# Optimization experiments

Measured on AMD Instinct MI355X. Metric: run time of the kernel, lower is better.

## Reference

```python
import jax, jax.numpy as jnp
import numpy as np

B, N, D, E, K = 4, 4096, 2048, 128, 8


def setup_inputs() -> dict:
    key = jax.random.key(0)
    kx, kw, kb = jax.random.split(key, 3)
    x = jax.random.normal(kx, (B, N, D), dtype=jnp.float32)
    # nn.Linear(input_dim, num_experts): weight [E, D], bias [E]
    bound = 1.0 / np.sqrt(D)
    W = jax.random.uniform(kw, (E, D), dtype=jnp.float32, minval=-bound, maxval=bound)
    b = jax.random.uniform(kb, (E,), dtype=jnp.float32, minval=-bound, maxval=bound)
    return {"x": x, "W": W, "b": b}


def reference(x, W, b):
    # gate logits: [B, N, E]
    gate_logits = jnp.einsum("bnd,ed->bne", x, W) + b
    # top-k over experts
    topk_values, topk_indices = jax.lax.top_k(gate_logits, K)  # [B,N,K]
    topk_gates = jax.nn.softmax(topk_values, axis=-1)          # [B,N,K]
    # scatter normalized gates back into dense [B,N,E]
    onehot = jax.nn.one_hot(topk_indices, E, dtype=topk_gates.dtype)  # [B,N,K,E]
    full_gates = jnp.einsum("bnke,bnk->bne", onehot, topk_gates)
    return full_gates, topk_indices
```

## Files before the change

kernel.cpp:

```cpp
#include <hip/hip_runtime.h>
#include <cfloat>

#define TOKENS 16384
#define DDIM   2048
#define NEXP   128
#define KTOP   8
#define MB     64
#define CH     64
#define NCH    (DDIM / CH)
#define NTHR   512

typedef float    f32x4 __attribute__((ext_vector_type(4)));
typedef _Float16 f16x8 __attribute__((ext_vector_type(8)));

#define WFRAG_N (8 * NCH * 2 * 64)

__device__ __forceinline__ unsigned short f16bits(float f) {
    _Float16 h = (_Float16)f;
    return __builtin_bit_cast(unsigned short, h);
}
__device__ __forceinline__ float f16tof(unsigned short u) {
    return (float)__builtin_bit_cast(_Float16, u);
}

__global__ __launch_bounds__(256, 1) void wfrag_kernel(
    const float* __restrict__ W, uint4* __restrict__ wf)
{
    int id   = blockIdx.x * 256 + threadIdx.x;
    int lane = id & 63;
    int ks   = (id >> 6) & 1;
    int c    = (id >> 7) & (NCH - 1);
    int eb   = id >> 12;
    int e    = eb * 16 + (lane & 15);
    int k0   = c * CH + ks * 32 + (lane >> 4) * 8;
    const float4* src = (const float4*)(W + (size_t)e * DDIM + k0);
    float4 a = src[0], bq = src[1];
    float v[8] = {a.x, a.y, a.z, a.w, bq.x, bq.y, bq.z, bq.w};
    unsigned hw[4], mw[4];
#pragma unroll
    for (int p = 0; p < 4; ++p) {
        unsigned short h0 = f16bits(v[2 * p]), h1 = f16bits(v[2 * p + 1]);
        unsigned short m0 = f16bits((v[2 * p]     - f16tof(h0)) * 4096.0f);
        unsigned short m1 = f16bits((v[2 * p + 1] - f16tof(h1)) * 4096.0f);
        hw[p] = (unsigned)h0 | ((unsigned)h1 << 16);
        mw[p] = (unsigned)m0 | ((unsigned)m1 << 16);
    }
    wf[id]           = make_uint4(hw[0], hw[1], hw[2], hw[3]);
    wf[WFRAG_N + id] = make_uint4(mw[0], mw[1], mw[2], mw[3]);
}

__device__ __forceinline__ void insert8(float (&vals)[8], int (&idxs)[8], float v, int e) {
    bool c[8];
#pragma unroll
    for (int p = 0; p < 8; ++p) c[p] = v > vals[p];
#pragma unroll
    for (int p = 7; p >= 1; --p) {
        vals[p] = c[p] ? (c[p - 1] ? vals[p - 1] : v) : vals[p];
        idxs[p] = c[p] ? (c[p - 1] ? idxs[p - 1] : e) : idxs[p];
    }
    vals[0] = c[0] ? v : vals[0];
    idxs[0] = c[0] ? e : idxs[0];
}

__device__ __forceinline__ void chunk_barrier() {
    asm volatile("s_waitcnt lgkmcnt(0)" ::: "memory");
    __builtin_amdgcn_sched_barrier(0);
    __builtin_amdgcn_s_barrier();
    __builtin_amdgcn_sched_barrier(0);
}

__global__ __launch_bounds__(NTHR, 1) void router_kernel(
    const float* __restrict__ x, const uint4* __restrict__ wf,
    const float* __restrict__ b, float* __restrict__ out_gates,
    float* __restrict__ out_idx)
{
    __shared__ __align__(16) char smem[52224];
    float* lg  = (float*)smem;
    float* plv = (float*)(smem + 33792);
    int*   pli = (int*)(smem + 43008);

    const int tid  = threadIdx.x;
    const int lane = tid & 63;
    const int wid  = tid >> 6;
    const int tok0 = blockIdx.x * MB;

    const uint4* WFH = wf;
    const uint4* WFM = wf + WFRAG_N;

    f32x4 acc1[4], acc2[4];
#pragma unroll
    for (int mf = 0; mf < 4; ++mf) {
        acc1[mf] = (f32x4){0.f, 0.f, 0.f, 0.f};
        acc2[mf] = (f32x4){0.f, 0.f, 0.f, 0.f};
    }

    const float4* x4 = (const float4*)x;
    const int xr0 = tid >> 4, xr1 = 32 + (tid >> 4), xq = tid & 15;
    const size_t xoff0 = (size_t)(tok0 + xr0) * (DDIM / 4) + xq;
    const size_t xoff1 = (size_t)(tok0 + xr1) * (DDIM / 4) + xq;
    const int xb0 = xr0 * 128 + (((xq >> 1) ^ (xr0 & 7)) << 4) + (xq & 1) * 8;
    const int xb1 = xr1 * 128 + (((xq >> 1) ^ (xr1 & 7)) << 4) + (xq & 1) * 8;

    float4 S0[2], S1[2], S2[2], S3[2], S4[2], S5[2], S6[2], S7[2];
    uint4  wA[4], wB[4];

    auto loadX = [&](int c, float4 (&S)[2]) {
        S[0] = x4[xoff0 + (size_t)c * 16];
        S[1] = x4[xoff1 + (size_t)c * 16];
    };
    auto loadW = [&](int c, uint4 (&wreg)[4]) {
#pragma unroll
        for (int ks = 0; ks < 2; ++ks) {
            int idx = ((wid * NCH + c) * 2 + ks) * 64 + lane;
            wreg[ks]     = WFH[idx];
            wreg[2 + ks] = WFM[idx];
        }
    };
    auto convertX = [&](const float4 (&sx)[2], char* ldsDst) {
#pragma unroll
        for (int r = 0; r < 2; ++r) {
            const float4 v = sx[r];
            unsigned short h0 = f16bits(v.x), h1 = f16bits(v.y);
            unsigned short h2 = f16bits(v.z), h3 = f16bits(v.w);
            unsigned short m0 = f16bits((v.x - f16tof(h0)) * 4096.0f);
            unsigned short m1 = f16bits((v.y - f16tof(h1)) * 4096.0f);
            unsigned short m2 = f16bits((v.z - f16tof(h2)) * 4096.0f);
            unsigned short m3 = f16bits((v.w - f16tof(h3)) * 4096.0f);
            uint2 hv = make_uint2((unsigned)h0 | ((unsigned)h1 << 16),
                                  (unsigned)h2 | ((unsigned)h3 << 16));
            uint2 mv = make_uint2((unsigned)m0 | ((unsigned)m1 << 16),
                                  (unsigned)m2 | ((unsigned)m3 << 16));
            const int byteoff = r ? xb1 : xb0;
            *(uint2*)(ldsDst + byteoff)         = hv;
            *(uint2*)(ldsDst + 16384 + byteoff) = mv;
        }
    };

    auto step = [&](int c, float4 (&Sload)[2], float4 (&Scvt)[2],
                    uint4 (&wCur)[4], uint4 (&wNext)[4],
                    char* bufCur, char* bufNext) {
        if (c + 8 < NCH) loadX(c + 8, Sload);
        if (c + 1 < NCH) loadW(c + 1, wNext);

#pragma unroll
        for (int ks = 0; ks < 2; ++ks) {
            f16x8 ah[4], am[4];
#pragma unroll
            for (int mf = 0; mf < 4; ++mf) {
                int row = 16 * mf + (lane & 15);
                int byteoff = row * 128 +
                    ((((ks << 2) | (lane >> 4)) ^ (row & 7)) << 4);
                ah[mf] = *(const f16x8*)(bufCur + byteoff);
                am[mf] = *(const f16x8*)(bufCur + 16384 + byteoff);
            }
            f16x8 wh = __builtin_bit_cast(f16x8, wCur[ks]);
            f16x8 wm = __builtin_bit_cast(f16x8, wCur[2 + ks]);
#pragma unroll
            for (int mf = 0; mf < 4; ++mf) {
                acc1[mf] = __builtin_amdgcn_mfma_f32_16x16x32_f16(
                    ah[mf], wh, acc1[mf], 0, 0, 0);
                acc2[mf] = __builtin_amdgcn_mfma_f32_16x16x32_f16(
                    ah[mf], wm, acc2[mf], 0, 0, 0);
                acc2[mf] = __builtin_amdgcn_mfma_f32_16x16x32_f16(
                    am[mf], wh, acc2[mf], 0, 0, 0);
            }
        }

        if (c + 1 < NCH) convertX(Scvt, bufNext);
        chunk_barrier();
    };

    loadX(0, S0);
    loadX(1, S1);
    loadW(0, wA);
    loadX(2, S2);
    loadX(3, S3);
    loadX(4, S4);
    loadX(5, S5);
    loadX(6, S6);
    loadX(7, S7);
    convertX(S0, smem);
    chunk_barrier();

    char* buf0 = smem;
    char* buf1 = smem + 8192;
    for (int cc = 0; cc < NCH; cc += 8) {
        step(cc,     S0, S1, wA, wB, buf0, buf1);
        step(cc + 1, S1, S2, wB, wA, buf1, buf0);
        step(cc + 2, S2, S3, wA, wB, buf0, buf1);
        step(cc + 3, S3, S4, wB, wA, buf1, buf0);
        step(cc + 4, S4, S5, wA, wB, buf0, buf1);
        step(cc + 5, S5, S6, wB, wA, buf1, buf0);
        step(cc + 6, S6, S7, wA, wB, buf0, buf1);
        step(cc + 7, S7, S0, wB, wA, buf1, buf0);
    }

    const float bb = b[wid * 16 + (lane & 15)];
#pragma unroll
    for (int mf = 0; mf < 4; ++mf)
#pragma unroll
        for (int r = 0; r < 4; ++r) {
            int t = 16 * mf + (lane >> 4) * 4 + r;
            int e = wid * 16 + (lane & 15);
            lg[t * 132 + e] =
                fmaf(acc2[mf][r], 0.000244140625f, acc1[mf][r]) + bb;
        }
    __syncthreads();

    if (tid < 256) {
        int tt = tid >> 2, p = tid & 3;
        float vals[8]; int idxs[8];
#pragma unroll
        for (int k = 0; k < 8; ++k) { vals[k] = -FLT_MAX; idxs[k] = 0; }
        const float* row = &lg[tt * 132 + p * 32];
        for (int q = 0; q < 32; ++q)
            insert8(vals, idxs, row[q], p * 32 + q);
#pragma unroll
        for (int k = 0; k < 8; ++k) {
            plv[tid * 9 + k] = vals[k];
            pli[tid * 9 + k] = idxs[k];
        }
    }
    __syncthreads();

    float g[8]; int fidx[8];
    const bool active = (tid < MB);
    if (active) {
        float vals[8]; int idxs[8];
#pragma unroll
        for (int k = 0; k < 8; ++k) { vals[k] = -FLT_MAX; idxs[k] = 0; }
        for (int p = 0; p < 4; ++p) {
#pragma unroll
            for (int k = 0; k < 8; ++k)
                insert8(vals, idxs, plv[(tid * 4 + p) * 9 + k], pli[(tid * 4 + p) * 9 + k]);
        }
        float mx = vals[0];
        float s = 0.0f;
#pragma unroll
        for (int k = 0; k < 8; ++k) { g[k] = __expf(vals[k] - mx); s += g[k]; }
        float inv = 1.0f / s;
#pragma unroll
        for (int k = 0; k < 8; ++k) { g[k] *= inv; fidx[k] = idxs[k]; }
#pragma unroll
        for (int k = 0; k < 8; ++k)
            out_idx[(size_t)(tok0 + tid) * KTOP + k] = (float)idxs[k];
    }
    for (int f = tid; f < MB * 132; f += NTHR) lg[f] = 0.0f;
    __syncthreads();

    if (active) {
#pragma unroll
        for (int k = 0; k < 8; ++k) lg[tid * 132 + fidx[k]] = g[k];
    }
    __syncthreads();

    for (int f = tid; f < MB * (NEXP / 4); f += NTHR) {
        int m = f >> 5, e4 = f & 31;
        float4 v = *(const float4*)&lg[m * 132 + e4 * 4];
        ((float4*)out_gates)[(size_t)(tok0 + m) * (NEXP / 4) + e4] = v;
    }
}

extern "C" void kernel_launch(void* const* d_in, const int* in_sizes, int n_in,
                              void* d_out, int out_size, void* d_ws, size_t ws_size,
                              hipStream_t stream) {
    const float* x = (const float*)d_in[0];
    const float* W = (const float*)d_in[1];
    const float* b = (const float*)d_in[2];

    float* out_gates = (float*)d_out;
    float* out_idx   = out_gates + (size_t)TOKENS * NEXP;

    uint4* wf = (uint4*)d_ws;

    wfrag_kernel<<<dim3(WFRAG_N / 256), dim3(256), 0, stream>>>(W, wf);
    router_kernel<<<dim3(TOKENS / MB), dim3(NTHR), 0, stream>>>(x, wf, b, out_gates, out_idx);
}
```

Baseline: 53.06 us.

## Split the D reduction across two blocks and combine partials in a separate kernel

Measured after the change: 62.25 us. 1.17x slower.

```diff
diff --git a/kernel.cpp b/kernel.cpp
--- a/kernel.cpp
+++ b/kernel.cpp
@@ -8,6 +8,7 @@
 #define MB     64
 #define CH     64
 #define NCH    (DDIM / CH)
+#define NCHH   (NCH / 2)
 #define NTHR   512
 
 typedef float    f32x4 __attribute__((ext_vector_type(4)));
@@ -69,20 +70,18 @@
     __builtin_amdgcn_sched_barrier(0);
 }
 
-__global__ __launch_bounds__(NTHR, 1) void router_kernel(
+__global__ __launch_bounds__(NTHR, 1) void router_split_kernel(
     const float* __restrict__ x, const uint4* __restrict__ wf,
-    const float* __restrict__ b, float* __restrict__ out_gates,
-    float* __restrict__ out_idx)
+    float* __restrict__ pl)
 {
-    __shared__ __align__(16) char smem[52224];
-    float* lg  = (float*)smem;
-    float* plv = (float*)(smem + 33792);
-    int*   pli = (int*)(smem + 43008);
+    __shared__ __align__(16) char smem[32768];
 
     const int tid  = threadIdx.x;
     const int lane = tid & 63;
     const int wid  = tid >> 6;
-    const int tok0 = blockIdx.x * MB;
+    const int bi   = blockIdx.x;
+    const int kh   = bi & 1;
+    const int tok0 = (bi >> 1) * MB;
 
     const uint4* WFH = wf;
     const uint4* WFM = wf + WFRAG_N;
@@ -96,22 +95,23 @@
 
     const float4* x4 = (const float4*)x;
     const int xr0 = tid >> 4, xr1 = 32 + (tid >> 4), xq = tid & 15;
-    const size_t xoff0 = (size_t)(tok0 + xr0) * (DDIM / 4) + xq;
-    const size_t xoff1 = (size_t)(tok0 + xr1) * (DDIM / 4) + xq;
+    const size_t xoff0 = (size_t)(tok0 + xr0) * (DDIM / 4) + (size_t)kh * NCHH * 16 + xq;
+    const size_t xoff1 = (size_t)(tok0 + xr1) * (DDIM / 4) + (size_t)kh * NCHH * 16 + xq;
     const int xb0 = xr0 * 128 + (((xq >> 1) ^ (xr0 & 7)) << 4) + (xq & 1) * 8;
     const int xb1 = xr1 * 128 + (((xq >> 1) ^ (xr1 & 7)) << 4) + (xq & 1) * 8;
 
     float4 S0[2], S1[2], S2[2], S3[2], S4[2], S5[2], S6[2], S7[2];
     uint4  wA[4], wB[4];
 
-    auto loadX = [&](int c, float4 (&S)[2]) {
-        S[0] = x4[xoff0 + (size_t)c * 16];
-        S[1] = x4[xoff1 + (size_t)c * 16];
-    };
-    auto loadW = [&](int c, uint4 (&wreg)[4]) {
+    auto loadX = [&](int cr, float4 (&S)[2]) {
+        S[0] = x4[xoff0 + (size_t)cr * 16];
+        S[1] = x4[xoff1 + (size_t)cr * 16];
+    };
+    auto loadW = [&](int cr, uint4 (&wreg)[4]) {
+        const int ca = kh * NCHH + cr;
 #pragma unroll
         for (int ks = 0; ks < 2; ++ks) {
-            int idx = ((wid * NCH + c) * 2 + ks) * 64 + lane;
+            int idx = ((wid * NCH + ca) * 2 + ks) * 64 + lane;
             wreg[ks]     = WFH[idx];
             wreg[2 + ks] = WFM[idx];
         }
@@ -136,11 +136,11 @@
         }
     };
 
-    auto step = [&](int c, float4 (&Sload)[2], float4 (&Scvt)[2],
+    auto step = [&](int cr, float4 (&Sload)[2], float4 (&Scvt)[2],
                     uint4 (&wCur)[4], uint4 (&wNext)[4],
                     char* bufCur, char* bufNext) {
-        if (c + 8 < NCH) loadX(c + 8, Sload);
-        if (c + 1 < NCH) loadW(c + 1, wNext);
+        if (cr + 8 < NCHH) loadX(cr + 8, Sload);
+        if (cr + 1 < NCHH) loadW(cr + 1, wNext);
 
 #pragma unroll
         for (int ks = 0; ks < 2; ++ks) {
@@ -166,19 +166,230 @@
             }
         }
 
+        if (cr + 1 < NCHH) convertX(Scvt, bufNext);
+        chunk_barrier();
+    };
+
+    loadX(0, S0); loadX(1, S1);
+    loadW(0, wA);
+    loadX(2, S2); loadX(3, S3);
+    loadX(4, S4); loadX(5, S5);
+    loadX(6, S6); loadX(7, S7);
+    convertX(S0, smem);
+    chunk_barrier();
+
+    char* buf0 = smem;
+    char* buf1 = smem + 8192;
+    for (int cc = 0; cc < NCHH; cc += 8) {
+        step(cc,     S0, S1, wA, wB, buf0, buf1);
+        step(cc + 1, S1, S2, wB, wA, buf1, buf0);
+        step(cc + 2, S2, S3, wA, wB, buf0, buf1);
+        step(cc + 3, S3, S4, wB, wA, buf1, buf0);
+        step(cc + 4, S4, S5, wA, wB, buf0, buf1);
+        step(cc + 5, S5, S6, wB, wA, buf1, buf0);
+        step(cc + 6, S6, S7, wA, wB, buf0, buf1);
+        step(cc + 7, S7, S0, wB, wA, buf1, buf0);
+    }
+
+    float* plh = pl + (size_t)kh * TOKENS * NEXP;
+#pragma unroll
+    for (int mf = 0; mf < 4; ++mf)
+#pragma unroll
+        for (int r = 0; r < 4; ++r) {
+            int t = 16 * mf + (lane >> 4) * 4 + r;
+            int e = wid * 16 + (lane & 15);
+            plh[(size_t)(tok0 + t) * NEXP + e] =
+                fmaf(acc2[mf][r], 0.000244140625f, acc1[mf][r]);
+        }
+}
+
+__global__ __launch_bounds__(NTHR, 1) void combine_kernel(
+    const float* __restrict__ pl, const float* __restrict__ b,
+    float* __restrict__ out_gates, float* __restrict__ out_idx)
+{
+    __shared__ __align__(16) char smem[52224];
+    float* lg  = (float*)smem;
+    float* plv = (float*)(smem + 33792);
+    int*   pli = (int*)(smem + 43008);
+
+    const int tid  = threadIdx.x;
+    const int tok0 = blockIdx.x * MB;
+
+    const float4* p0 = (const float4*)pl;
+    const float4* p1 = (const float4*)(pl + (size_t)TOKENS * NEXP);
+    const float4* b4 = (const float4*)b;
+
+    for (int f = tid; f < MB * (NEXP / 4); f += NTHR) {
+        int m = f >> 5, e4 = f & 31;
+        size_t gi = (size_t)(tok0 + m) * (NEXP / 4) + e4;
+        float4 v0 = p0[gi], v1 = p1[gi], bb = b4[e4];
+        float4 v;
+        v.x = v0.x + v1.x + bb.x;
+        v.y = v0.y + v1.y + bb.y;
+        v.z = v0.z + v1.z + bb.z;
+        v.w = v0.w + v1.w + bb.w;
+        *(float4*)&lg[m * 132 + e4 * 4] = v;
+    }
+    __syncthreads();
+
+    if (tid < 256) {
+        int tt = tid >> 2, p = tid & 3;
+        float vals[8]; int idxs[8];
+#pragma unroll
+        for (int k = 0; k < 8; ++k) { vals[k] = -FLT_MAX; idxs[k] = 0; }
+        const float* row = &lg[tt * 132 + p * 32];
+        for (int q = 0; q < 32; ++q)
+            insert8(vals, idxs, row[q], p * 32 + q);
+#pragma unroll
+        for (int k = 0; k < 8; ++k) {
+            plv[tid * 9 + k] = vals[k];
+            pli[tid * 9 + k] = idxs[k];
+        }
+    }
+    __syncthreads();
+
+    float g[8]; int fidx[8];
+    const bool active = (tid < MB);
+    if (active) {
+        float vals[8]; int idxs[8];
+#pragma unroll
+        for (int k = 0; k < 8; ++k) { vals[k] = -FLT_MAX; idxs[k] = 0; }
+        for (int p = 0; p < 4; ++p) {
+#pragma unroll
+            for (int k = 0; k < 8; ++k)
+                insert8(vals, idxs, plv[(tid * 4 + p) * 9 + k], pli[(tid * 4 + p) * 9 + k]);
+        }
+        float mx = vals[0];
+        float s = 0.0f;
+#pragma unroll
+        for (int k = 0; k < 8; ++k) { g[k] = __expf(vals[k] - mx); s += g[k]; }
+        float inv = 1.0f / s;
+#pragma unroll
+        for (int k = 0; k < 8; ++k) { g[k] *= inv; fidx[k] = idxs[k]; }
+#pragma unroll
+        for (int k = 0; k < 8; ++k)
+            out_idx[(size_t)(tok0 + tid) * KTOP + k] = (float)idxs[k];
+    }
+    for (int f = tid; f < MB * 132; f += NTHR) lg[f] = 0.0f;
+    __syncthreads();
+
+    if (active) {
+#pragma unroll
+        for (int k = 0; k < 8; ++k) lg[tid * 132 + fidx[k]] = g[k];
+    }
+    __syncthreads();
+
+    for (int f = tid; f < MB * (NEXP / 4); f += NTHR) {
+        int m = f >> 5, e4 = f & 31;
+        float4 v = *(const float4*)&lg[m * 132 + e4 * 4];
+        ((float4*)out_gates)[(size_t)(tok0 + m) * (NEXP / 4) + e4] = v;
+    }
+}
+
+__global__ __launch_bounds__(NTHR, 1) void router_kernel(
+    const float* __restrict__ x, const uint4* __restrict__ wf,
+    const float* __restrict__ b, float* __restrict__ out_gates,
+    float* __restrict__ out_idx)
+{
+    __shared__ __align__(16) char smem[52224];
+    float* lg  = (float*)smem;
+    float* plv = (float*)(smem + 33792);
+    int*   pli = (int*)(smem + 43008);
+
+    const int tid  = threadIdx.x;
+    const int lane = tid & 63;
+    const int wid  = tid >> 6;
+    const int tok0 = blockIdx.x * MB;
+
+    const uint4* WFH = wf;
+    const uint4* WFM = wf + WFRAG_N;
+
+    f32x4 acc1[4], acc2[4];
+#pragma unroll
+    for (int mf = 0; mf < 4; ++mf) {
+        acc1[mf] = (f32x4){0.f, 0.f, 0.f, 0.f};
+        acc2[mf] = (f32x4){0.f, 0.f, 0.f, 0.f};
+    }
+
+    const float4* x4 = (const float4*)x;
+    const int xr0 = tid >> 4, xr1 = 32 + (tid >> 4), xq = tid & 15;
+    const size_t xoff0 = (size_t)(tok0 + xr0) * (DDIM / 4) + xq;
+    const size_t xoff1 = (size_t)(tok0 + xr1) * (DDIM / 4) + xq;
+    const int xb0 = xr0 * 128 + (((xq >> 1) ^ (xr0 & 7)) << 4) + (xq & 1) * 8;
+    const int xb1 = xr1 * 128 + (((xq >> 1) ^ (xr1 & 7)) << 4) + (xq & 1) * 8;
+
+    float4 S0[2], S1[2], S2[2], S3[2], S4[2], S5[2], S6[2], S7[2];
+    uint4  wA[4], wB[4];
+
+    auto loadX = [&](int c, float4 (&S)[2]) {
+        S[0] = x4[xoff0 + (size_t)c * 16];
+        S[1] = x4[xoff1 + (size_t)c * 16];
+    };
+    auto loadW = [&](int c, uint4 (&wreg)[4]) {
+#pragma unroll
+        for (int ks = 0; ks < 2; ++ks) {
+            int idx = ((wid * NCH + c) * 2 + ks) * 64 + lane;
+            wreg[ks]     = WFH[idx];
+            wreg[2 + ks] = WFM[idx];
+        }
+    };
+    auto convertX = [&](const float4 (&sx)[2], char* ldsDst) {
+#pragma unroll
+        for (int r = 0; r < 2; ++r) {
+            const float4 v = sx[r];
+            unsigned short h0 = f16bits(v.x), h1 = f16bits(v.y);
+            unsigned short h2 = f16bits(v.z), h3 = f16bits(v.w);
+            unsigned short m0 = f16bits((v.x - f16tof(h0)) * 4096.0f);
+            unsigned short m1 = f16bits((v.y - f16tof(h1)) * 4096.0f);
+            unsigned short m2 = f16bits((v.z - f16tof(h2)) * 4096.0f);
+            unsigned short m3 = f16bits((v.w - f16tof(h3)) * 4096.0f);
+            uint2 hv = make_uint2((unsigned)h0 | ((unsigned)h1 << 16),
+                                  (unsigned)h2 | ((unsigned)h3 << 16));
+            uint2 mv = make_uint2((unsigned)m0 | ((unsigned)m1 << 16),
+                                  (unsigned)m2 | ((unsigned)m3 << 16));
+            const int byteoff = r ? xb1 : xb0;
+            *(uint2*)(ldsDst + byteoff)         = hv;
+            *(uint2*)(ldsDst + 16384 + byteoff) = mv;
+        }
+    };
+
+    auto step = [&](int c, float4 (&Sload)[2], float4 (&Scvt)[2],
+                    uint4 (&wCur)[4], uint4 (&wNext)[4],
+                    char* bufCur, char* bufNext) {
+        if (c + 8 < NCH) loadX(c + 8, Sload);
+        if (c + 1 < NCH) loadW(c + 1, wNext);
+#pragma unroll
+        for (int ks = 0; ks < 2; ++ks) {
+            f16x8 ah[4], am[4];
+#pragma unroll
+            for (int mf = 0; mf < 4; ++mf) {
+                int row = 16 * mf + (lane & 15);
+                int byteoff = row * 128 +
+                    ((((ks << 2) | (lane >> 4)) ^ (row & 7)) << 4);
+                ah[mf] = *(const f16x8*)(bufCur + byteoff);
+                am[mf] = *(const f16x8*)(bufCur + 16384 + byteoff);
+            }
+            f16x8 wh = __builtin_bit_cast(f16x8, wCur[ks]);
+            f16x8 wm = __builtin_bit_cast(f16x8, wCur[2 + ks]);
+#pragma unroll
+            for (int mf = 0; mf < 4; ++mf) {
+                acc1[mf] = __builtin_amdgcn_mfma_f32_16x16x32_f16(
+                    ah[mf], wh, acc1[mf], 0, 0, 0);
+                acc2[mf] = __builtin_amdgcn_mfma_f32_16x16x32_f16(
+                    ah[mf], wm, acc2[mf], 0, 0, 0);
+                acc2[mf] = __builtin_amdgcn_mfma_f32_16x16x32_f16(
+                    am[mf], wh, acc2[mf], 0, 0, 0);
+            }
+        }
         if (c + 1 < NCH) convertX(Scvt, bufNext);
         chunk_barrier();
     };
 
-    loadX(0, S0);
-    loadX(1, S1);
+    loadX(0, S0); loadX(1, S1);
     loadW(0, wA);
-    loadX(2, S2);
-    loadX(3, S3);
-    loadX(4, S4);
-    loadX(5, S5);
-    loadX(6, S6);
-    loadX(7, S7);
+    loadX(2, S2); loadX(3, S3);
+    loadX(4, S4); loadX(5, S5);
+    loadX(6, S6); loadX(7, S7);
     convertX(S0, smem);
     chunk_barrier();
 
@@ -272,7 +483,16 @@
     float* out_idx   = out_gates + (size_t)TOKENS * NEXP;
 
     uint4* wf = (uint4*)d_ws;
+    const size_t wf_bytes = (size_t)2 * WFRAG_N * sizeof(uint4);
+    const size_t pl_bytes = (size_t)2 * TOKENS * NEXP * sizeof(float);
 
     wfrag_kernel<<<dim3(WFRAG_N / 256), dim3(256), 0, stream>>>(W, wf);
-    router_kernel<<<dim3(TOKENS / MB), dim3(NTHR), 0, stream>>>(x, wf, b, out_gates, out_idx);
-}
+
+    if (ws_size >= wf_bytes + pl_bytes) {
+        float* pl = (float*)((char*)d_ws + wf_bytes);
+        router_split_kernel<<<dim3(2 * TOKENS / MB), dim3(NTHR), 0, stream>>>(x, wf, pl);
+        combine_kernel<<<dim3(TOKENS / MB), dim3(NTHR), 0, stream>>>(pl, b, out_gates, out_idx);
+    } else {
+        router_kernel<<<dim3(TOKENS / MB), dim3(NTHR), 0, stream>>>(x, wf, b, out_gates, out_idx);
+    }
+}
```
